# Optimization experiments

Measured on AMD Instinct MI355X. Metric: run time of the kernel, lower is better.

Reference implementation:

```python
import jax, jax.numpy as jnp
import numpy as np

B, N, L, F = 8, 256, 48, 96

def setup_inputs() -> dict:
    key = jax.random.key(0)
    k1, k2 = jax.random.split(key)
    x = jax.random.normal(k1, (B, N, N, L), dtype=jnp.float32)
    w = jax.random.normal(k2, (15, L, F), dtype=jnp.float32) * 0.05  # 'random_normal' init
    return {"x": x, "w": w}

def reference(x, w):
    # x: [B, N, N, L], w: [15, L, F]
    Bn, Nn, _, Ln = x.shape
    totsum = jnp.einsum('bijl->bl', x)          # [B, L]
    trace  = jnp.einsum('biil->bl', x)          # [B, L]
    diag   = jnp.einsum('biil->bil', x)         # [B, N, L]
    rowsum = jnp.einsum('bijl->bil', x)         # sum over j -> [B, N, L] (index i)
    colsum = jnp.einsum('bijl->bjl', x)         # sum over i -> [B, N, L] (index j)

    # Diagonal-placed terms (res0..res4): delta_ij * (node part + scalar part)
    diag_node = (jnp.einsum('bil,lf->bif', diag,   w[0])
               + jnp.einsum('bil,lf->bif', rowsum, w[1])
               + jnp.einsum('bil,lf->bif', colsum, w[2]))          # [B, N, F]
    diag_scal = trace @ w[3] + totsum @ w[4]                        # [B, F]
    eye = jnp.eye(Nn, dtype=x.dtype)
    out = (eye[None, :, :, None] * diag_node[:, :, None, :]
         + eye[None, :, :, None] * diag_scal[:, None, None, :])    # [B, N, N, F]

    # Broadcast over i (res5..res7: vector indexed by j)
    bj = (jnp.einsum('bjl,lf->bjf', diag,   w[5])
        + jnp.einsum('bjl,lf->bjf', rowsum, w[6])
        + jnp.einsum('bjl,lf->bjf', colsum, w[7]))                 # [B, N, F]
    out = out + bj[:, None, :, :]

    # Broadcast over j (res8..res10: vector indexed by i)
    bi = (jnp.einsum('bil,lf->bif', diag,   w[8])
        + jnp.einsum('bil,lf->bif', rowsum, w[9])
        + jnp.einsum('bil,lf->bif', colsum, w[10]))                # [B, N, F]
    out = out + bi[:, :, None, :]

    # Dense terms: transpose (res11) and identity (res12)
    out = out + jnp.einsum('bijl,lf->bjif', x, w[11])
    out = out + jnp.einsum('bijl,lf->bijf', x, w[12])

    # Global scalar broadcasts (res13, res14)
    scal = trace @ w[13] + totsum @ w[14]                           # [B, F]
    out = out + scal[:, None, None, :]
    return out
```

## Files before the change

kernel.cpp:

```cpp
#include <hip/hip_runtime.h>

#define Bx 8
#define Nx 256
#define Lx 48
#define Fx 96
#define KP 104

typedef __attribute__((ext_vector_type(8))) short bf16x8;
typedef __attribute__((ext_vector_type(4))) float f32x4;

__device__ __forceinline__ unsigned short f2bf(float f) {
    unsigned int u = __float_as_uint(f);
    u += 0x7fffu + ((u >> 16) & 1u);
    return (unsigned short)(u >> 16);
}
__device__ __forceinline__ unsigned int pack2(float a, float b) {
    return (unsigned int)f2bf(a) | ((unsigned int)f2bf(b) << 16);
}

__global__ __launch_bounds__(192) void k_row(const float* __restrict__ x,
                                             float* __restrict__ rowsum,
                                             float* __restrict__ diagv) {
    const int blk = blockIdx.x;
    const int t = threadIdx.x;
    const int l = t % Lx;
    const int g = t / Lx;
    __shared__ float red[192];
    const size_t base = (size_t)blk * Nx * Lx;
    float acc = 0.f;
    for (int j = g; j < Nx; j += 4)
        acc += x[base + (size_t)j * Lx + l];
    red[t] = acc;
    __syncthreads();
    if (g == 0)
        rowsum[(size_t)blk * Lx + l] = red[l] + red[48 + l] + red[96 + l] + red[144 + l];
    if (t < Lx)
        diagv[(size_t)blk * Lx + t] = x[base + (size_t)(blk & 255) * Lx + t];
}

__global__ __launch_bounds__(256) void k_col(const float* __restrict__ x,
                                             float* __restrict__ colsum) {
    const int blk = blockIdx.x;
    const int is = blk & 7;
    const int jc = (blk >> 3) & 15;
    const int b  = blk >> 7;
    const int t = threadIdx.x;
    const size_t cb = (size_t)b * Nx * Nx * Lx + (size_t)jc * 16 * Lx;
    float a0 = 0.f, a1 = 0.f, a2 = 0.f;
    for (int ii = 0; ii < 32; ++ii) {
        const int i = is * 32 + ii;
        const float* p = x + cb + (size_t)i * Nx * Lx;
        a0 += p[t];
        a1 += p[t + 256];
        a2 += p[t + 512];
    }
    float* c = colsum + ((size_t)b * Nx + jc * 16) * Lx;
    atomicAdd(c + t, a0);
    atomicAdd(c + t + 256, a1);
    atomicAdd(c + t + 512, a2);
}

__global__ __launch_bounds__(64) void k1b_trace(const float* __restrict__ rowsum,
                                                const float* __restrict__ diagv,
                                                float* __restrict__ trace,
                                                float* __restrict__ totsum) {
    const int b = blockIdx.x;
    const int l = threadIdx.x;
    if (l >= Lx) return;
    float tr = 0.f, ts = 0.f;
    for (int i = 0; i < Nx; ++i) {
        const size_t idx = (size_t)(b * Nx + i) * Lx + l;
        tr += diagv[idx];
        ts += rowsum[idx];
    }
    trace[b * Lx + l]  = tr;
    totsum[b * Lx + l] = ts;
}

__global__ __launch_bounds__(128) void k2_vectors(const float* __restrict__ w,
                                                  const float* __restrict__ rowsum,
                                                  const float* __restrict__ colsum,
                                                  const float* __restrict__ diagv,
                                                  const float* __restrict__ trace,
                                                  const float* __restrict__ totsum,
                                                  float* __restrict__ add_i,
                                                  float* __restrict__ add_j,
                                                  float* __restrict__ add_d) {
    const int blk = blockIdx.x;
    const int b = blk >> 8;
    const int f = threadIdx.x;
    if (f >= Fx) return;

    const float* dP  = diagv  + (size_t)blk * Lx;
    const float* rP  = rowsum + (size_t)blk * Lx;
    const float* cP  = colsum + (size_t)blk * Lx;
    const float* trP = trace  + b * Lx;
    const float* tsP = totsum + b * Lx;

    float ai = 0.f, aj = 0.f, ad = 0.f;
    #pragma unroll 4
    for (int l = 0; l < Lx; ++l) {
        const float d  = dP[l];
        const float r  = rP[l];
        const float c  = cP[l];
        const float tr = trP[l];
        const float ts = tsP[l];
        const float* wl = w + (size_t)l * Fx + f;
        ad = fmaf(d,  wl[0  * Lx * Fx], ad);
        ad = fmaf(r,  wl[1  * Lx * Fx], ad);
        ad = fmaf(c,  wl[2  * Lx * Fx], ad);
        ad = fmaf(tr, wl[3  * Lx * Fx], ad);
        ad = fmaf(ts, wl[4  * Lx * Fx], ad);
        aj = fmaf(d,  wl[5  * Lx * Fx], aj);
        aj = fmaf(r,  wl[6  * Lx * Fx], aj);
        aj = fmaf(c,  wl[7  * Lx * Fx], aj);
        ai = fmaf(d,  wl[8  * Lx * Fx], ai);
        ai = fmaf(r,  wl[9  * Lx * Fx], ai);
        ai = fmaf(c,  wl[10 * Lx * Fx], ai);
        ai = fmaf(tr, wl[13 * Lx * Fx], ai);
        ai = fmaf(ts, wl[14 * Lx * Fx], ai);
    }
    add_i[(size_t)blk * Fx + f] = ai;
    add_j[(size_t)blk * Fx + f] = aj;
    add_d[(size_t)blk * Fx + f] = ad;
}

__global__ __launch_bounds__(256) void k_w(const float* __restrict__ w,
                                           unsigned short* __restrict__ wt) {
    const int idx = blockIdx.x * 256 + threadIdx.x;
    if (idx >= Fx * KP) return;
    const int f = idx / KP, kk = idx % KP;
    float v = 0.f;
    if (kk < 48)      v = w[12 * Lx * Fx + kk * Fx + f];
    else if (kk < 96) v = w[11 * Lx * Fx + (kk - 48) * Fx + f];
    wt[idx] = f2bf(v);
}

__global__ __launch_bounds__(256) void k3_mfma(const float* __restrict__ x,
                                               const unsigned short* __restrict__ wt,
                                               const float* __restrict__ add_i,
                                               const float* __restrict__ add_j,
                                               const float* __restrict__ add_d,
                                               float* __restrict__ out) {
    __shared__ unsigned short Al[64 * KP];
    __shared__ unsigned short Bl[96 * KP];
    const int idx = blockIdx.x;
    const int b   = blockIdx.y;
    const int p   = idx >> 6;
    const int io  = idx & 63;
    int It, Jt;
    if (p < 4)      { It = 0; Jt = p; }
    else if (p < 7) { It = 1; Jt = p - 3; }
    else if (p < 9) { It = 2; Jt = p - 5; }
    else            { It = 3; Jt = 3; }
    const int i  = It * 64 + io;
    const int J  = Jt * 64;
    const int bi = b * Nx + i;
    const int t  = threadIdx.x;

    {
        const uint4* src = (const uint4*)wt;
        uint4* dst = (uint4*)Bl;
        #pragma unroll
        for (int it = 0; it < 5; ++it) {
            const int k = t + it * 256;
            if (k < (96 * KP * 2) / 16) dst[k] = src[k];
        }
    }
    {
        const int r = t >> 2, q = t & 3;
        const float* pij = x + ((size_t)bi * Nx + J + r) * Lx;
        const float* pji = x + ((size_t)(b * Nx + J + r) * Nx + i) * Lx;
        unsigned int* arow = (unsigned int*)Al + r * (KP / 2);
        #pragma unroll
        for (int e = 0; e < 3; ++e) {
            const float4 v = *(const float4*)(pij + q * 4 + e * 16);
            arow[q * 2 + e * 8 + 0] = pack2(v.x, v.y);
            arow[q * 2 + e * 8 + 1] = pack2(v.z, v.w);
        }
        #pragma unroll
        for (int e = 0; e < 3; ++e) {
            const float4 v = *(const float4*)(pji + q * 4 + e * 16);
            arow[24 + q * 2 + e * 8 + 0] = pack2(v.x, v.y);
            arow[24 + q * 2 + e * 8 + 1] = pack2(v.z, v.w);
        }
    }
    __syncthreads();

    const int wave = t >> 6, lane = t & 63;
    const int lm = lane & 15, quad = lane >> 4;
    const int m0 = wave * 16;

    const float* aiP = add_i + (size_t)bi * Fx;
    const float* ajP = add_j + (size_t)bi * Fx;
    const float* adP = add_d + (size_t)bi * Fx;
    float* outP = out + (size_t)bi * Nx * Fx;

    const int npass = (It == Jt) ? 1 : 2;
    for (int pass = 0; pass < npass; ++pass) {
        bf16x8 afr[3];
        #pragma unroll
        for (int ks = 0; ks < 3; ++ks) {
            int off = ks * 32 + quad * 8;
            if (pass) off = (off < 48) ? off + 48 : off - 48;
            afr[ks] = *(const bf16x8*)(Al + (m0 + lm) * KP + off);
        }
        #pragma unroll
        for (int nt = 0; nt < 6; ++nt) {
            f32x4 c = {0.f, 0.f, 0.f, 0.f};
            #pragma unroll
            for (int ks = 0; ks < 3; ++ks) {
                const bf16x8 bfr = *(const bf16x8*)(Bl + (nt * 16 + lm) * KP + ks * 32 + quad * 8);
                c = __builtin_amdgcn_mfma_f32_16x16x32_bf16(afr[ks], bfr, c, 0, 0, 0);
            }
            const int f = nt * 16 + lm;
            if (pass == 0) {
                const float ai = aiP[f];
                #pragma unroll
                for (int reg = 0; reg < 4; ++reg) {
                    const int j = J + m0 + quad * 4 + reg;
                    float v = c[reg] + ai + add_j[((size_t)(b * Nx) + j) * Fx + f];
                    if (j == i) v += adP[f];
                    outP[(size_t)j * Fx + f] = v;
                }
            } else {
                const float aj = ajP[f];
                #pragma unroll
                for (int reg = 0; reg < 4; ++reg) {
                    const int row = J + m0 + quad * 4 + reg;
                    float v = c[reg] + aj + add_i[((size_t)(b * Nx) + row) * Fx + f];
                    out[((size_t)(b * Nx + row) * Nx + i) * Fx + f] = v;
                }
            }
        }
    }
}

extern "C" void kernel_launch(void* const* d_in, const int* in_sizes, int n_in,
                              void* d_out, int out_size, void* d_ws, size_t ws_size,
                              hipStream_t stream) {
    const float* x = (const float*)d_in[0];
    const float* w = (const float*)d_in[1];
    float* out = (float*)d_out;

    float* ws      = (float*)d_ws;
    float* rowsum  = ws;
    float* colsum  = rowsum + (size_t)Bx * Nx * Lx;
    float* diagv   = colsum + (size_t)Bx * Nx * Lx;
    float* trace   = diagv  + (size_t)Bx * Nx * Lx;
    float* totsum  = trace  + (size_t)Bx * Lx;
    float* add_i   = totsum + (size_t)Bx * Lx;
    float* add_j   = add_i  + (size_t)Bx * Nx * Fx;
    float* add_d   = add_j  + (size_t)Bx * Nx * Fx;
    unsigned short* wtbf = (unsigned short*)(add_d + (size_t)Bx * Nx * Fx);

    k_row<<<Bx * Nx, 192, 0, stream>>>(x, rowsum, diagv);
    hipMemsetAsync(colsum, 0, (size_t)Bx * Nx * Lx * sizeof(float), stream);
    k_col<<<Bx * 16 * 8, 256, 0, stream>>>(x, colsum);
    k1b_trace<<<Bx, 64, 0, stream>>>(rowsum, diagv, trace, totsum);
    k2_vectors<<<Bx * Nx, 128, 0, stream>>>(w, rowsum, colsum, diagv, trace, totsum,
                                            add_i, add_j, add_d);
    k_w<<<(Fx * KP + 255) / 256, 256, 0, stream>>>(w, wtbf);
    dim3 g3(640, Bx);
    k3_mfma<<<g3, 256, 0, stream>>>(x, wtbf, add_i, add_j, add_d, out);
}
```

Measured before the change: 391.3 us.

## Fuse reduction kernels, batch vector GEMV, swizzle MFMA grid, nontemporal stores

Merges row/column sums, diagonal extraction, trace/total reduction (now via atomics) and weight bf16 packing into one launch, cutting several kernel launches and an extra pass over rowsum/diagv. The vector kernel now handles two nodes per thread and hoists the scalar trace/totsum terms, so weight loads are reused. The main MFMA kernel remaps block indices, shares B fragments between the direct and transposed passes, uses a hardware packed bf16 convert, and writes output with nontemporal stores. Atomic float accumulation for trace/totsum changes summation order, and the memset now has to cover those buffers as well.

Result: faster. 378.7 us (-3.2%).

```diff
diff --git a/kernel.cpp b/kernel.cpp
--- a/kernel.cpp
+++ b/kernel.cpp
@@ -14,70 +14,73 @@
     u += 0x7fffu + ((u >> 16) & 1u);
     return (unsigned short)(u >> 16);
 }
-__device__ __forceinline__ unsigned int pack2(float a, float b) {
-    return (unsigned int)f2bf(a) | ((unsigned int)f2bf(b) << 16);
-}
-
-__global__ __launch_bounds__(192) void k_row(const float* __restrict__ x,
-                                             float* __restrict__ rowsum,
-                                             float* __restrict__ diagv) {
+__device__ __forceinline__ unsigned int cvt_pk_bf16(float a, float b) {
+    unsigned int r;
+    asm("v_cvt_pk_bf16_f32 %0, %1, %2" : "=v"(r) : "v"(a), "v"(b));
+    return r;
+}
+
+__global__ __launch_bounds__(192) void kA_fused(const float* __restrict__ x,
+                                                const float* __restrict__ w,
+                                                float* __restrict__ rowsum,
+                                                float* __restrict__ colsum,
+                                                float* __restrict__ diagv,
+                                                float* __restrict__ trace,
+                                                float* __restrict__ totsum,
+                                                unsigned short* __restrict__ wt) {
     const int blk = blockIdx.x;
     const int t = threadIdx.x;
-    const int l = t % Lx;
-    const int g = t / Lx;
-    __shared__ float red[192];
-    const size_t base = (size_t)blk * Nx * Lx;
-    float acc = 0.f;
-    for (int j = g; j < Nx; j += 4)
-        acc += x[base + (size_t)j * Lx + l];
-    red[t] = acc;
-    __syncthreads();
-    if (g == 0)
-        rowsum[(size_t)blk * Lx + l] = red[l] + red[48 + l] + red[96 + l] + red[144 + l];
-    if (t < Lx)
-        diagv[(size_t)blk * Lx + t] = x[base + (size_t)(blk & 255) * Lx + t];
-}
-
-__global__ __launch_bounds__(256) void k_col(const float* __restrict__ x,
-                                             float* __restrict__ colsum) {
-    const int blk = blockIdx.x;
-    const int is = blk & 7;
-    const int jc = (blk >> 3) & 15;
-    const int b  = blk >> 7;
-    const int t = threadIdx.x;
-    const size_t cb = (size_t)b * Nx * Nx * Lx + (size_t)jc * 16 * Lx;
-    float a0 = 0.f, a1 = 0.f, a2 = 0.f;
-    for (int ii = 0; ii < 32; ++ii) {
-        const int i = is * 32 + ii;
-        const float* p = x + cb + (size_t)i * Nx * Lx;
-        a0 += p[t];
-        a1 += p[t + 256];
-        a2 += p[t + 512];
-    }
-    float* c = colsum + ((size_t)b * Nx + jc * 16) * Lx;
-    atomicAdd(c + t, a0);
-    atomicAdd(c + t + 256, a1);
-    atomicAdd(c + t + 512, a2);
-}
-
-__global__ __launch_bounds__(64) void k1b_trace(const float* __restrict__ rowsum,
-                                                const float* __restrict__ diagv,
-                                                float* __restrict__ trace,
-                                                float* __restrict__ totsum) {
-    const int b = blockIdx.x;
-    const int l = threadIdx.x;
-    if (l >= Lx) return;
-    float tr = 0.f, ts = 0.f;
-    for (int i = 0; i < Nx; ++i) {
-        const size_t idx = (size_t)(b * Nx + i) * Lx + l;
-        tr += diagv[idx];
-        ts += rowsum[idx];
-    }
-    trace[b * Lx + l]  = tr;
-    totsum[b * Lx + l] = ts;
-}
-
-__global__ __launch_bounds__(128) void k2_vectors(const float* __restrict__ w,
+    if (blk < Bx * Nx) {
+        __shared__ float red[192];
+        const int l = t % Lx;
+        const int g = t / Lx;
+        const int b = blk >> 8;
+        const size_t base = (size_t)blk * Nx * Lx;
+        float acc = 0.f;
+        for (int j = g; j < Nx; j += 4)
+            acc += x[base + (size_t)j * Lx + l];
+        red[t] = acc;
+        __syncthreads();
+        if (g == 0) {
+            const float rs = red[l] + red[48 + l] + red[96 + l] + red[144 + l];
+            rowsum[(size_t)blk * Lx + l] = rs;
+            atomicAdd(totsum + b * Lx + l, rs);
+        }
+        if (t < Lx) {
+            const float dv = x[base + (size_t)(blk & 255) * Lx + t];
+            diagv[(size_t)blk * Lx + t] = dv;
+            atomicAdd(trace + b * Lx + t, dv);
+        }
+    } else if (blk < Bx * Nx + 1024) {
+        const int c  = blk - Bx * Nx;
+        const int is = c & 7;
+        const int jc = (c >> 3) & 15;
+        const int b  = c >> 7;
+        const size_t cb = (size_t)b * Nx * Nx * Lx + (size_t)jc * 16 * Lx;
+        float a0 = 0.f, a1 = 0.f, a2 = 0.f, a3 = 0.f;
+        for (int ii = 0; ii < 32; ++ii) {
+            const float* p = x + cb + (size_t)(is * 32 + ii) * Nx * Lx;
+            a0 += p[t];
+            a1 += p[t + 192];
+            a2 += p[t + 384];
+            a3 += p[t + 576];
+        }
+        float* cp = colsum + ((size_t)b * Nx + jc * 16) * Lx;
+        atomicAdd(cp + t,       a0);
+        atomicAdd(cp + t + 192, a1);
+        atomicAdd(cp + t + 384, a2);
+        atomicAdd(cp + t + 576, a3);
+    } else {
+        const int idx = (blk - (Bx * Nx + 1024)) * 192 + t;
+        const int f = idx / KP, kk = idx % KP;
+        float v = 0.f;
+        if (kk < 48)      v = w[12 * Lx * Fx + kk * Fx + f];
+        else if (kk < 96) v = w[11 * Lx * Fx + (kk - 48) * Fx + f];
+        wt[idx] = f2bf(v);
+    }
+}
+
+__global__ __launch_bounds__(192) void k2_vectors(const float* __restrict__ w,
                                                   const float* __restrict__ rowsum,
                                                   const float* __restrict__ colsum,
                                                   const float* __restrict__ diagv,
@@ -87,53 +90,50 @@
                                                   float* __restrict__ add_j,
                                                   float* __restrict__ add_d) {
     const int blk = blockIdx.x;
-    const int b = blk >> 8;
-    const int f = threadIdx.x;
-    if (f >= Fx) return;
-
-    const float* dP  = diagv  + (size_t)blk * Lx;
-    const float* rP  = rowsum + (size_t)blk * Lx;
-    const float* cP  = colsum + (size_t)blk * Lx;
+    const int t = threadIdx.x;
+    const int f  = t % Fx;
+    const int nh = t / Fx;
+    const int b  = blk >> 6;
+    const int nb = b * Nx + (blk & 63) * 4 + nh * 2;
     const float* trP = trace  + b * Lx;
     const float* tsP = totsum + b * Lx;
 
-    float ai = 0.f, aj = 0.f, ad = 0.f;
-    #pragma unroll 4
+    float ai[2] = {0.f, 0.f}, aj[2] = {0.f, 0.f}, ad[2] = {0.f, 0.f};
+    float sd = 0.f, si = 0.f;
     for (int l = 0; l < Lx; ++l) {
-        const float d  = dP[l];
-        const float r  = rP[l];
-        const float c  = cP[l];
-        const float tr = trP[l];
-        const float ts = tsP[l];
         const float* wl = w + (size_t)l * Fx + f;
-        ad = fmaf(d,  wl[0  * Lx * Fx], ad);
-        ad = fmaf(r,  wl[1  * Lx * Fx], ad);
-        ad = fmaf(c,  wl[2  * Lx * Fx], ad);
-        ad = fmaf(tr, wl[3  * Lx * Fx], ad);
-        ad = fmaf(ts, wl[4  * Lx * Fx], ad);
-        aj = fmaf(d,  wl[5  * Lx * Fx], aj);
-        aj = fmaf(r,  wl[6  * Lx * Fx], aj);
-        aj = fmaf(c,  wl[7  * Lx * Fx], aj);
-        ai = fmaf(d,  wl[8  * Lx * Fx], ai);
-        ai = fmaf(r,  wl[9  * Lx * Fx], ai);
-        ai = fmaf(c,  wl[10 * Lx * Fx], ai);
-        ai = fmaf(tr, wl[13 * Lx * Fx], ai);
-        ai = fmaf(ts, wl[14 * Lx * Fx], ai);
-    }
-    add_i[(size_t)blk * Fx + f] = ai;
-    add_j[(size_t)blk * Fx + f] = aj;
-    add_d[(size_t)blk * Fx + f] = ad;
-}
-
-__global__ __launch_bounds__(256) void k_w(const float* __restrict__ w,
-                                           unsigned short* __restrict__ wt) {
-    const int idx = blockIdx.x * 256 + threadIdx.x;
-    if (idx >= Fx * KP) return;
-    const int f = idx / KP, kk = idx % KP;
-    float v = 0.f;
-    if (kk < 48)      v = w[12 * Lx * Fx + kk * Fx + f];
-    else if (kk < 96) v = w[11 * Lx * Fx + (kk - 48) * Fx + f];
-    wt[idx] = f2bf(v);
+        const float w0  = wl[0];
+        const float w1  = wl[1  * Lx * Fx];
+        const float w2  = wl[2  * Lx * Fx];
+        const float w3  = wl[3  * Lx * Fx];
+        const float w4  = wl[4  * Lx * Fx];
+        const float w5  = wl[5  * Lx * Fx];
+        const float w6  = wl[6  * Lx * Fx];
+        const float w7  = wl[7  * Lx * Fx];
+        const float w8  = wl[8  * Lx * Fx];
+        const float w9  = wl[9  * Lx * Fx];
+        const float w10 = wl[10 * Lx * Fx];
+        const float w13 = wl[13 * Lx * Fx];
+        const float w14 = wl[14 * Lx * Fx];
+        const float tr = trP[l], ts = tsP[l];
+        sd = fmaf(tr, w3,  sd); sd = fmaf(ts, w4,  sd);
+        si = fmaf(tr, w13, si); si = fmaf(ts, w14, si);
+        #pragma unroll
+        for (int nn = 0; nn < 2; ++nn) {
+            const size_t ix = (size_t)(nb + nn) * Lx + l;
+            const float d = diagv[ix], r = rowsum[ix], c = colsum[ix];
+            ad[nn] = fmaf(d, w0, ad[nn]); ad[nn] = fmaf(r, w1, ad[nn]); ad[nn] = fmaf(c, w2,  ad[nn]);
+            aj[nn] = fmaf(d, w5, aj[nn]); aj[nn] = fmaf(r, w6, aj[nn]); aj[nn] = fmaf(c, w7,  aj[nn]);
+            ai[nn] = fmaf(d, w8, ai[nn]); ai[nn] = fmaf(r, w9, ai[nn]); ai[nn] = fmaf(c, w10, ai[nn]);
+        }
+    }
+    #pragma unroll
+    for (int nn = 0; nn < 2; ++nn) {
+        const size_t idx = (size_t)(nb + nn) * Fx + f;
+        add_d[idx] = ad[nn] + sd;
+        add_j[idx] = aj[nn];
+        add_i[idx] = ai[nn] + si;
+    }
 }
 
 __global__ __launch_bounds__(256) void k3_mfma(const float* __restrict__ x,
@@ -144,10 +144,11 @@
                                                float* __restrict__ out) {
     __shared__ unsigned short Al[64 * KP];
     __shared__ unsigned short Bl[96 * KP];
-    const int idx = blockIdx.x;
-    const int b   = blockIdx.y;
-    const int p   = idx >> 6;
-    const int io  = idx & 63;
+    const int rawx = blockIdx.x;
+    const int idx  = (rawx & 7) * 80 + (rawx >> 3);
+    const int b    = blockIdx.y;
+    const int p    = idx >> 6;
+    const int io   = idx & 63;
     int It, Jt;
     if (p < 4)      { It = 0; Jt = p; }
     else if (p < 7) { It = 1; Jt = p - 3; }
@@ -175,14 +176,14 @@
         #pragma unroll
         for (int e = 0; e < 3; ++e) {
             const float4 v = *(const float4*)(pij + q * 4 + e * 16);
-            arow[q * 2 + e * 8 + 0] = pack2(v.x, v.y);
-            arow[q * 2 + e * 8 + 1] = pack2(v.z, v.w);
+            arow[q * 2 + e * 8 + 0] = cvt_pk_bf16(v.x, v.y);
+            arow[q * 2 + e * 8 + 1] = cvt_pk_bf16(v.z, v.w);
         }
         #pragma unroll
         for (int e = 0; e < 3; ++e) {
             const float4 v = *(const float4*)(pji + q * 4 + e * 16);
-            arow[24 + q * 2 + e * 8 + 0] = pack2(v.x, v.y);
-            arow[24 + q * 2 + e * 8 + 1] = pack2(v.z, v.w);
+            arow[24 + q * 2 + e * 8 + 0] = cvt_pk_bf16(v.x, v.y);
+            arow[24 + q * 2 + e * 8 + 1] = cvt_pk_bf16(v.z, v.w);
         }
     }
     __syncthreads();
@@ -190,47 +191,63 @@
     const int wave = t >> 6, lane = t & 63;
     const int lm = lane & 15, quad = lane >> 4;
     const int m0 = wave * 16;
+    const bool offd = (It != Jt);
 
     const float* aiP = add_i + (size_t)bi * Fx;
     const float* ajP = add_j + (size_t)bi * Fx;
     const float* adP = add_d + (size_t)bi * Fx;
     float* outP = out + (size_t)bi * Nx * Fx;
 
-    const int npass = (It == Jt) ? 1 : 2;
-    for (int pass = 0; pass < npass; ++pass) {
-        bf16x8 afr[3];
+    bf16x8 afr0[3], afr1[3];
+    #pragma unroll
+    for (int ks = 0; ks < 3; ++ks) {
+        const int off = ks * 32 + quad * 8;
+        afr0[ks] = *(const bf16x8*)(Al + (m0 + lm) * KP + off);
+    }
+    if (offd) {
         #pragma unroll
         for (int ks = 0; ks < 3; ++ks) {
-            int off = ks * 32 + quad * 8;
-            if (pass) off = (off < 48) ? off + 48 : off - 48;
-            afr[ks] = *(const bf16x8*)(Al + (m0 + lm) * KP + off);
-        }
-        #pragma unroll
-        for (int nt = 0; nt < 6; ++nt) {
-            f32x4 c = {0.f, 0.f, 0.f, 0.f};
+            const int off  = ks * 32 + quad * 8;
+            const int offm = (off < 48) ? off + 48 : off - 48;
+            afr1[ks] = *(const bf16x8*)(Al + (m0 + lm) * KP + offm);
+        }
+    }
+
+    const int jbase = J + m0 + quad * 4;
+    #pragma unroll
+    for (int nt = 0; nt < 6; ++nt) {
+        bf16x8 bfr[3];
+        #pragma unroll
+        for (int ks = 0; ks < 3; ++ks)
+            bfr[ks] = *(const bf16x8*)(Bl + (nt * 16 + lm) * KP + ks * 32 + quad * 8);
+        const int f = nt * 16 + lm;
+
+        f32x4 c0 = {0.f, 0.f, 0.f, 0.f};
+        #pragma unroll
+        for (int ks = 0; ks < 3; ++ks)
+            c0 = __builtin_amdgcn_mfma_f32_16x16x32_bf16(afr0[ks], bfr[ks], c0, 0, 0, 0);
+        {
+            const float ai = aiP[f];
+            const float* ajRow = add_j + ((size_t)(b * Nx) + jbase) * Fx + f;
             #pragma unroll
-            for (int ks = 0; ks < 3; ++ks) {
-                const bf16x8 bfr = *(const bf16x8*)(Bl + (nt * 16 + lm) * KP + ks * 32 + quad * 8);
-                c = __builtin_amdgcn_mfma_f32_16x16x32_bf16(afr[ks], bfr, c, 0, 0, 0);
+            for (int reg = 0; reg < 4; ++reg) {
+                float v = c0[reg] + ai + ajRow[(size_t)reg * Fx];
+                if (!offd && (jbase + reg == i)) v += adP[f];
+                __builtin_nontemporal_store(v, outP + (size_t)(jbase + reg) * Fx + f);
             }
-            const int f = nt * 16 + lm;
-            if (pass == 0) {
-                const float ai = aiP[f];
-                #pragma unroll
-                for (int reg = 0; reg < 4; ++reg) {
-                    const int j = J + m0 + quad * 4 + reg;
-                    float v = c[reg] + ai + add_j[((size_t)(b * Nx) + j) * Fx + f];
-                    if (j == i) v += adP[f];
-                    outP[(size_t)j * Fx + f] = v;
-                }
-            } else {
-                const float aj = ajP[f];
-                #pragma unroll
-                for (int reg = 0; reg < 4; ++reg) {
-                    const int row = J + m0 + quad * 4 + reg;
-                    float v = c[reg] + aj + add_i[((size_t)(b * Nx) + row) * Fx + f];
-                    out[((size_t)(b * Nx + row) * Nx + i) * Fx + f] = v;
-                }
+        }
+        if (offd) {
+            f32x4 c1 = {0.f, 0.f, 0.f, 0.f};
+            #pragma unroll
+            for (int ks = 0; ks < 3; ++ks)
+                c1 = __builtin_amdgcn_mfma_f32_16x16x32_bf16(afr1[ks], bfr[ks], c1, 0, 0, 0);
+            const float aj = ajP[f];
+            const float* aiRow = add_i + ((size_t)(b * Nx) + jbase) * Fx + f;
+            float* op = out + ((size_t)(b * Nx + jbase) * Nx + i) * Fx + f;
+            #pragma unroll
+            for (int reg = 0; reg < 4; ++reg) {
+                const float v = c1[reg] + aj + aiRow[(size_t)reg * Fx];
+                __builtin_nontemporal_store(v, op + (size_t)reg * Nx * Fx);
             }
         }
     }
@@ -244,23 +261,21 @@
     float* out = (float*)d_out;
 
     float* ws      = (float*)d_ws;
-    float* rowsum  = ws;
-    float* colsum  = rowsum + (size_t)Bx * Nx * Lx;
-    float* diagv   = colsum + (size_t)Bx * Nx * Lx;
-    float* trace   = diagv  + (size_t)Bx * Nx * Lx;
+    float* colsum  = ws;
+    float* trace   = colsum + (size_t)Bx * Nx * Lx;
     float* totsum  = trace  + (size_t)Bx * Lx;
-    float* add_i   = totsum + (size_t)Bx * Lx;
+    float* rowsum  = totsum + (size_t)Bx * Lx;
+    float* diagv   = rowsum + (size_t)Bx * Nx * Lx;
+    float* add_i   = diagv  + (size_t)Bx * Nx * Lx;
     float* add_j   = add_i  + (size_t)Bx * Nx * Fx;
     float* add_d   = add_j  + (size_t)Bx * Nx * Fx;
     unsigned short* wtbf = (unsigned short*)(add_d + (size_t)Bx * Nx * Fx);
 
-    k_row<<<Bx * Nx, 192, 0, stream>>>(x, rowsum, diagv);
-    hipMemsetAsync(colsum, 0, (size_t)Bx * Nx * Lx * sizeof(float), stream);
-    k_col<<<Bx * 16 * 8, 256, 0, stream>>>(x, colsum);
-    k1b_trace<<<Bx, 64, 0, stream>>>(rowsum, diagv, trace, totsum);
-    k2_vectors<<<Bx * Nx, 128, 0, stream>>>(w, rowsum, colsum, diagv, trace, totsum,
-                                            add_i, add_j, add_d);
-    k_w<<<(Fx * KP + 255) / 256, 256, 0, stream>>>(w, wtbf);
+    hipMemsetAsync(ws, 0, ((size_t)Bx * Nx * Lx + 2 * Bx * Lx) * sizeof(float), stream);
+    kA_fused<<<Bx * Nx + 1024 + 52, 192, 0, stream>>>(x, w, rowsum, colsum, diagv,
+                                                      trace, totsum, wtbf);
+    k2_vectors<<<512, 192, 0, stream>>>(w, rowsum, colsum, diagv, trace, totsum,
+                                        add_i, add_j, add_d);
     dim3 g3(640, Bx);
     k3_mfma<<<g3, 256, 0, stream>>>(x, wtbf, add_i, add_j, add_d, out);
 }
```
